# Optimization experiments

Measured on AMD Instinct MI355X. Metric: run time of the kernel, lower is better.

The kernel has to match this reference:

```python
import jax, jax.numpy as jnp
import numpy as np
from jax import lax

R = 0.1  # radius_graph radius (matches init kwarg r)


def setup_inputs() -> dict:
    key = jax.random.key(0)
    ks = jax.random.split(key, 16)
    B, O, K, F = 8, 4, 512, 3
    H = 128
    def lin(k, fan_in, fan_out):
        return jax.random.normal(k, (fan_in, fan_out), jnp.float32) / np.sqrt(fan_in)
    return {
        "points": jax.random.uniform(ks[0], (B, O, K, F), jnp.float32),
        "com": jax.random.normal(ks[1], (B, O, 3), jnp.float32),
        "com_vel": jax.random.normal(ks[2], (B, O, 3), jnp.float32),
        "angle": jax.random.normal(ks[3], (B, O, 3), jnp.float32),
        "angle_vel": jax.random.normal(ks[4], (B, O, 3), jnp.float32),
        "padding": jnp.ones((B, O, K), jnp.float32),
        "W0": lin(ks[5], 2 * F, H), "b0": jnp.zeros((H,), jnp.float32),
        "W1": lin(ks[6], H, H), "b1": jnp.zeros((H,), jnp.float32),
        "W2": lin(ks[7], H, H), "b2": jnp.zeros((H,), jnp.float32),
        "Wfc": lin(ks[8], H, 2 * F), "bfc": jnp.zeros((2 * F,), jnp.float32),
        "knn": 8,
        "pred_len": 10,
    }


def reference(points, com, com_vel, angle, angle_vel, padding,
              W0, b0, W1, b1, W2, b2, Wfc, bfc, knn, pred_len):
    B, O, K, F = points.shape
    N = O * K  # nodes per batch element
    pad = padding.reshape(B, N)                       # float mask [B,N]
    padb = pad > 0
    edge_ok = padb[:, :, None] & padb[:, None, :]     # valid src & dst
    not_self = ~jnp.eye(N, dtype=bool)
    eye = jnp.eye(N, dtype=points.dtype)

    states0 = jnp.concatenate([points, jnp.zeros_like(points)], -1).reshape(B, N, 2 * F)

    def gconv(a_hat, dinv, x, W, b):
        # GCNConv: out_i = sum_j A_hat[ij] d_i^-1/2 d_j^-1/2 (xW)_j + b
        h = (x @ W) * dinv[..., None]
        return jnp.einsum('bij,bjd->bid', a_hat, h) * dinv[..., None] + b

    def step(states, _):
        pos = states[..., :3]                         # [B,N,3]
        d2 = jnp.sum((pos[:, :, None, :] - pos[:, None, :, :]) ** 2, -1)
        adj = (d2 < R * R) & not_self & edge_ok       # radius_graph + padding mask
        a_hat = lax.stop_gradient(adj.astype(states.dtype) + eye)  # self-loops (all nodes)
        dinv = lax.rsqrt(a_hat.sum(-1))               # deg >= 1
        x = jax.nn.relu(gconv(a_hat, dinv, states, W0, b0))
        x = jax.nn.relu(gconv(a_hat, dinv, x, W1, b1))
        x = jax.nn.relu(gconv(a_hat, dinv, x, W2, b2))
        res = x @ Wfc + bfc
        new = states + res * pad[..., None]
        return new, new

    _, traj = lax.scan(step, states0, None, length=pred_len)
    traj = jnp.concatenate([states0[:, None], jnp.swapaxes(traj, 0, 1)], axis=1)
    return traj.reshape(B, pred_len + 1, O, K, 2 * F)[..., :3]
```

## Files before the change

### kernel.cpp

```cpp
#include <hip/hip_runtime.h>
#include <math.h>

#define BB 8
#define NN 2048
#define HH 128
#define NSEG 8
#define SEGJ 256
#define SEGCAP 12
#define MAXNBR (NSEG*SEGCAP)
#define PREDL 10
#define TSTRIDE (NN*3)
#define OUT_BSTRIDE ((PREDL+1)*NN*3)

__global__ __launch_bounds__(256) void k_init(const float* __restrict__ points,
                                              float* __restrict__ states,
                                              float* __restrict__ out) {
    int idx = blockIdx.x * 256 + threadIdx.x;
    if (idx >= BB * NN) return;
    int b = idx >> 11;
    int n = idx & 2047;
    float px = points[idx * 3 + 0];
    float py = points[idx * 3 + 1];
    float pz = points[idx * 3 + 2];
    float* s = states + (size_t)idx * 6;
    s[0] = px; s[1] = py; s[2] = pz; s[3] = 0.f; s[4] = 0.f; s[5] = 0.f;
    float* o = out + (size_t)b * OUT_BSTRIDE + n * 3;
    o[0] = px; o[1] = py; o[2] = pz;
}

__global__ __launch_bounds__(256, 2) void k_adj(const float* __restrict__ states,
                                                float* __restrict__ xs0,
                                                float* __restrict__ dinv,
                                                int* __restrict__ nbr,
                                                int* __restrict__ cntN) {
    const float R2c = 0.01f;
    int b = blockIdx.x & 7;
    int tile = blockIdx.x >> 3;
    __shared__ float4 pos[NN];
    __shared__ int degs[256];
    __shared__ unsigned short jb[256][SEGCAP];
    const float* sb = states + (size_t)b * NN * 6;
    for (int j = threadIdx.x; j < NN; j += 256) {
        const float* r = sb + j * 6;
        pos[j] = make_float4(r[0], r[1], r[2], 0.f);
    }
    __syncthreads();
    int node = threadIdx.x & 31;
    int seg  = threadIdx.x >> 5;
    int i = tile * 32 + node;
    int gi = b * NN + i;
    float4 pi = pos[i];
    int cnt = 0;
    int j0 = seg * SEGJ;
#pragma unroll 4
    for (int j = j0; j < j0 + SEGJ; ++j) {
        float4 pj = pos[j];
        float dx = pi.x - pj.x;
        float dy = pi.y - pj.y;
        float dz = pi.z - pj.z;
        float d2 = __fadd_rn(__fadd_rn(__fmul_rn(dx, dx), __fmul_rn(dy, dy)),
                             __fmul_rn(dz, dz));
        if (d2 < R2c && j != i) {
            if (cnt < SEGCAP) jb[threadIdx.x][cnt] = (unsigned short)j;
            cnt++;
        }
    }
    if (cnt > SEGCAP) cnt = SEGCAP;
    degs[threadIdx.x] = cnt;
    __syncthreads();
    int off = 0;
    for (int s = 0; s < seg; ++s) off += degs[s * 32 + node];
    int base = gi * MAXNBR + off;
    for (int k = 0; k < cnt; ++k) nbr[base + k] = (int)jb[threadIdx.x][k];
    if (seg == NSEG - 1) {
        int tot = off + cnt;
        cntN[gi] = tot;
        float di = (float)(1.0 / sqrt((double)(1 + tot)));
        dinv[gi] = di;
        const float* srow = sb + (size_t)i * 6;
        float* xr = xs0 + (size_t)gi * 6;
#pragma unroll
        for (int c = 0; c < 6; ++c) xr[c] = di * srow[c];
    }
}

__global__ __launch_bounds__(256, 2) void k_l0(const float* __restrict__ xs0,
                                               const float* __restrict__ dinv,
                                               const int* __restrict__ nbr,
                                               const int* __restrict__ cntN,
                                               const float* __restrict__ W0,
                                               const float* __restrict__ b0,
                                               float* __restrict__ xs1) {
    int b = blockIdx.x & 7;
    int tile = blockIdx.x >> 3;
    int node = threadIdx.x >> 3;
    int part = threadIdx.x & 7;
    int i = tile * 32 + node;
    int gi = b * NN + i;
    float g[6];
    {
        const float* sr = xs0 + (size_t)gi * 6;
        float2 a0 = *(const float2*)sr;
        float2 a1 = *(const float2*)(sr + 2);
        float2 a2 = *(const float2*)(sr + 4);
        g[0] = a0.x; g[1] = a0.y; g[2] = a1.x; g[3] = a1.y; g[4] = a2.x; g[5] = a2.y;
    }
    int cnt = cntN[gi];
    const int* nb = nbr + gi * MAXNBR;
    for (int k = 0; k < cnt; ++k) {
        int j = nb[k];
        const float* xr = xs0 + (size_t)(b * NN + j) * 6;
        float2 v0 = *(const float2*)xr;
        float2 v1 = *(const float2*)(xr + 2);
        float2 v2 = *(const float2*)(xr + 4);
        g[0] += v0.x; g[1] += v0.y; g[2] += v1.x;
        g[3] += v1.y; g[4] += v2.x; g[5] += v2.y;
    }
    float di = dinv[gi];
#pragma unroll
    for (int c = 0; c < 6; ++c) g[c] *= di;
    int c0 = part * 16;
    float y[16];
#pragma unroll
    for (int r = 0; r < 4; ++r) {
        float4 bv = *(const float4*)(b0 + c0 + r * 4);
        y[r * 4 + 0] = bv.x; y[r * 4 + 1] = bv.y; y[r * 4 + 2] = bv.z; y[r * 4 + 3] = bv.w;
    }
#pragma unroll
    for (int k = 0; k < 6; ++k) {
        float u = g[k];
        const float* wr = W0 + k * HH + c0;
#pragma unroll
        for (int r = 0; r < 4; ++r) {
            float4 w = *(const float4*)(wr + r * 4);
            y[r * 4 + 0] = fmaf(u, w.x, y[r * 4 + 0]);
            y[r * 4 + 1] = fmaf(u, w.y, y[r * 4 + 1]);
            y[r * 4 + 2] = fmaf(u, w.z, y[r * 4 + 2]);
            y[r * 4 + 3] = fmaf(u, w.w, y[r * 4 + 3]);
        }
    }
    float* xo = xs1 + (size_t)gi * HH + c0;
#pragma unroll
    for (int r = 0; r < 4; ++r) {
        float4 v;
        v.x = di * fmaxf(y[r * 4 + 0], 0.f);
        v.y = di * fmaxf(y[r * 4 + 1], 0.f);
        v.z = di * fmaxf(y[r * 4 + 2], 0.f);
        v.w = di * fmaxf(y[r * 4 + 3], 0.f);
        *(float4*)(xo + r * 4) = v;
    }
}

__device__ __forceinline__ void gather_into_lds(const float* __restrict__ xin,
                                                const float* __restrict__ dinv,
                                                const int* __restrict__ nbr,
                                                const int* __restrict__ cntN,
                                                int b, int tile,
                                                float (*uS)[HH + 4]) {
    const int node = threadIdx.x >> 3;
    const int part = threadIdx.x & 7;
    const int i = tile * 32 + node;
    const int gi = b * NN + i;
    const int c0 = part * 16;
    float acc[16];
    const float* xs = xin + (size_t)gi * HH + c0;
#pragma unroll
    for (int r = 0; r < 4; ++r) *(float4*)&acc[r * 4] = *(const float4*)(xs + r * 4);
    const int cnt = cntN[gi];
    const int* nb = nbr + gi * MAXNBR;
    for (int k = 0; k < cnt; ++k) {
        const int j = nb[k];
        const float* xr = xin + (size_t)(b * NN + j) * HH + c0;
#pragma unroll
        for (int r = 0; r < 4; ++r) {
            float v[4];
            *(float4*)v = *(const float4*)(xr + r * 4);
            acc[r * 4 + 0] += v[0]; acc[r * 4 + 1] += v[1];
            acc[r * 4 + 2] += v[2]; acc[r * 4 + 3] += v[3];
        }
    }
    const float di = dinv[gi];
#pragma unroll
    for (int r = 0; r < 4; ++r) {
        float4 o;
        o.x = acc[r * 4 + 0] * di; o.y = acc[r * 4 + 1] * di;
        o.z = acc[r * 4 + 2] * di; o.w = acc[r * 4 + 3] * di;
        *(float4*)&uS[node][c0 + r * 4] = o;
    }
}

__device__ __forceinline__ void gemm_panel(const float (*uS)[HH + 4],
                                           const float* __restrict__ wbuf,
                                           int p, int n0, int cA,
                                           float y0[8], float y1[8]) {
#pragma unroll 2
    for (int r = 0; r < 32; r += 4) {
        float ua[4], ub[4];
        *(float4*)ua = *(const float4*)(&uS[n0][p * 32 + r]);
        *(float4*)ub = *(const float4*)(&uS[n0 + 1][p * 32 + r]);
        const float* wrow = wbuf + r * HH + cA;
#pragma unroll
        for (int q = 0; q < 4; ++q) {
            float4 wa = *(const float4*)(wrow + q * HH);
            float4 wb = *(const float4*)(wrow + q * HH + 64);
            float u0 = ua[q], u1 = ub[q];
            y0[0] = fmaf(u0, wa.x, y0[0]); y0[1] = fmaf(u0, wa.y, y0[1]);
            y0[2] = fmaf(u0, wa.z, y0[2]); y0[3] = fmaf(u0, wa.w, y0[3]);
            y0[4] = fmaf(u0, wb.x, y0[4]); y0[5] = fmaf(u0, wb.y, y0[5]);
            y0[6] = fmaf(u0, wb.z, y0[6]); y0[7] = fmaf(u0, wb.w, y0[7]);
            y1[0] = fmaf(u1, wa.x, y1[0]); y1[1] = fmaf(u1, wa.y, y1[1]);
            y1[2] = fmaf(u1, wa.z, y1[2]); y1[3] = fmaf(u1, wa.w, y1[3]);
            y1[4] = fmaf(u1, wb.x, y1[4]); y1[5] = fmaf(u1, wb.y, y1[5]);
            y1[6] = fmaf(u1, wb.z, y1[6]); y1[7] = fmaf(u1, wb.w, y1[7]);
        }
    }
}

__global__ __launch_bounds__(256, 3) void k_mid(const float* __restrict__ xin,
                                                const float* __restrict__ dinv,
                                                const int* __restrict__ nbr,
                                                const int* __restrict__ cntN,
                                                const float* __restrict__ W,
                                                const float* __restrict__ bias,
                                                float* __restrict__ xout) {
    __shared__ __align__(16) float uS[32][HH + 4];
    __shared__ __align__(16) float wS[2][32 * HH];
    int b = blockIdx.x & 7;
    int tile = blockIdx.x >> 3;
    int t = threadIdx.x;
    const float4* Wf4 = (const float4*)W;
    float4 wreg[4];
#pragma unroll
    for (int q = 0; q < 4; ++q) wreg[q] = Wf4[t + q * 256];
    gather_into_lds(xin, dinv, nbr, cntN, b, tile, uS);
    {
        float4* ws4 = (float4*)wS[0];
#pragma unroll
        for (int q = 0; q < 4; ++q) ws4[t + q * 256] = wreg[q];
    }
    __syncthreads();
    int cb = t & 15, ng = t >> 4;
    int n0 = ng * 2, cA = cb * 4;
    float y0[8], y1[8];
    {
        float4 bv0 = *(const float4*)(bias + cA);
        float4 bv1 = *(const float4*)(bias + cA + 64);
        y0[0] = bv0.x; y0[1] = bv0.y; y0[2] = bv0.z; y0[3] = bv0.w;
        y0[4] = bv1.x; y0[5] = bv1.y; y0[6] = bv1.z; y0[7] = bv1.w;
#pragma unroll
        for (int r = 0; r < 8; ++r) y1[r] = y0[r];
    }
#pragma unroll
    for (int p = 0; p < 4; ++p) {
        if (p < 3) {
#pragma unroll
            for (int q = 0; q < 4; ++q) wreg[q] = Wf4[(p + 1) * 1024 + t + q * 256];
        }
        gemm_panel(uS, wS[p & 1], p, n0, cA, y0, y1);
        if (p < 3) {
            float4* ws4 = (float4*)wS[1 - (p & 1)];
#pragma unroll
            for (int q = 0; q < 4; ++q) ws4[t + q * 256] = wreg[q];
            __syncthreads();
        }
    }
    int g0 = b * NN + tile * 32 + n0;
    float di0 = dinv[g0], di1 = dinv[g0 + 1];
    float* o0 = xout + (size_t)g0 * HH + cA;
    float* o1 = o0 + HH;
    float4 va, vb;
    va.x = di0 * fmaxf(y0[0], 0.f); va.y = di0 * fmaxf(y0[1], 0.f);
    va.z = di0 * fmaxf(y0[2], 0.f); va.w = di0 * fmaxf(y0[3], 0.f);
    vb.x = di0 * fmaxf(y0[4], 0.f); vb.y = di0 * fmaxf(y0[5], 0.f);
    vb.z = di0 * fmaxf(y0[6], 0.f); vb.w = di0 * fmaxf(y0[7], 0.f);
    *(float4*)o0 = va; *(float4*)(o0 + 64) = vb;
    va.x = di1 * fmaxf(y1[0], 0.f); va.y = di1 * fmaxf(y1[1], 0.f);
    va.z = di1 * fmaxf(y1[2], 0.f); va.w = di1 * fmaxf(y1[3], 0.f);
    vb.x = di1 * fmaxf(y1[4], 0.f); vb.y = di1 * fmaxf(y1[5], 0.f);
    vb.z = di1 * fmaxf(y1[6], 0.f); vb.w = di1 * fmaxf(y1[7], 0.f);
    *(float4*)o1 = va; *(float4*)(o1 + 64) = vb;
}

__global__ __launch_bounds__(256, 3) void k_last(const float* __restrict__ xin,
                                                 const float* __restrict__ dinv,
                                                 const int* __restrict__ nbr,
                                                 const int* __restrict__ cntN,
                                                 const float* __restrict__ W2,
                                                 const float* __restrict__ b2,
                                                 const float* __restrict__ Wfc,
                                                 const float* __restrict__ bfc,
                                                 const float* __restrict__ padding,
                                                 float* __restrict__ states,
                                                 float* __restrict__ outt) {
    __shared__ __align__(16) float uS[32][HH + 4];
    __shared__ __align__(16) float wS[2][32 * HH];
    int b = blockIdx.x & 7;
    int tile = blockIdx.x >> 3;
    int t = threadIdx.x;
    const float4* Wf4 = (const float4*)W2;
    float4 wreg[4];
#pragma unroll
    for (int q = 0; q < 4; ++q) wreg[q] = Wf4[t + q * 256];
    gather_into_lds(xin, dinv, nbr, cntN, b, tile, uS);
    {
        float4* ws4 = (float4*)wS[0];
#pragma unroll
        for (int q = 0; q < 4; ++q) ws4[t + q * 256] = wreg[q];
    }
    __syncthreads();
    int cb = t & 15, ng = t >> 4;
    int n0 = ng * 2, cA = cb * 4;
    float y0[8], y1[8];
    {
        float4 bv0 = *(const float4*)(b2 + cA);
        float4 bv1 = *(const float4*)(b2 + cA + 64);
        y0[0] = bv0.x; y0[1] = bv0.y; y0[2] = bv0.z; y0[3] = bv0.w;
        y0[4] = bv1.x; y0[5] = bv1.y; y0[6] = bv1.z; y0[7] = bv1.w;
#pragma unroll
        for (int r = 0; r < 8; ++r) y1[r] = y0[r];
    }
#pragma unroll
    for (int p = 0; p < 4; ++p) {
        if (p < 3) {
#pragma unroll
            for (int q = 0; q < 4; ++q) wreg[q] = Wf4[(p + 1) * 1024 + t + q * 256];
        }
        gemm_panel(uS, wS[p & 1], p, n0, cA, y0, y1);
        if (p < 3) {
            float4* ws4 = (float4*)wS[1 - (p & 1)];
#pragma unroll
            for (int q = 0; q < 4; ++q) ws4[t + q * 256] = wreg[q];
            __syncthreads();
        }
    }
    __syncthreads();
    float* y3  = wS[0];
    float* wfc = wS[1];
#pragma unroll
    for (int q = 0; q < 3; ++q) wfc[t + q * 256] = Wfc[t + q * 256];
    {
        float4 v;
        v.x = fmaxf(y0[0], 0.f); v.y = fmaxf(y0[1], 0.f);
        v.z = fmaxf(y0[2], 0.f); v.w = fmaxf(y0[3], 0.f);
        *(float4*)&y3[n0 * HH + cA] = v;
        v.x = fmaxf(y0[4], 0.f); v.y = fmaxf(y0[5], 0.f);
        v.z = fmaxf(y0[6], 0.f); v.w = fmaxf(y0[7], 0.f);
        *(float4*)&y3[n0 * HH + cA + 64] = v;
        v.x = fmaxf(y1[0], 0.f); v.y = fmaxf(y1[1], 0.f);
        v.z = fmaxf(y1[2], 0.f); v.w = fmaxf(y1[3], 0.f);
        *(float4*)&y3[(n0 + 1) * HH + cA] = v;
        v.x = fmaxf(y1[4], 0.f); v.y = fmaxf(y1[5], 0.f);
        v.z = fmaxf(y1[6], 0.f); v.w = fmaxf(y1[7], 0.f);
        *(float4*)&y3[(n0 + 1) * HH + cA + 64] = v;
    }
    __syncthreads();
    if (t < 192) {
        int n = t / 6;
        int c = t - n * 6;
        float r = bfc[c];
        for (int k = 0; k < HH; k += 4) {
            float yv[4];
            *(float4*)yv = *(const float4*)&y3[n * HH + k];
            r = fmaf(yv[0], wfc[(k + 0) * 6 + c], r);
            r = fmaf(yv[1], wfc[(k + 1) * 6 + c], r);
            r = fmaf(yv[2], wfc[(k + 2) * 6 + c], r);
            r = fmaf(yv[3], wfc[(k + 3) * 6 + c], r);
        }
        int i = tile * 32 + n;
        int gi = b * NN + i;
        float pv = padding[b * NN + i];
        float s = states[(size_t)gi * 6 + c] + r * pv;
        states[(size_t)gi * 6 + c] = s;
        if (c < 3) outt[(size_t)b * OUT_BSTRIDE + i * 3 + c] = s;
    }
}

extern "C" void kernel_launch(void* const* d_in, const int* in_sizes, int n_in,
                              void* d_out, int out_size, void* d_ws, size_t ws_size,
                              hipStream_t stream) {
    (void)in_sizes; (void)n_in; (void)out_size; (void)ws_size;
    const float* points  = (const float*)d_in[0];
    const float* padding = (const float*)d_in[5];
    const float* W0  = (const float*)d_in[6];
    const float* b0  = (const float*)d_in[7];
    const float* W1  = (const float*)d_in[8];
    const float* b1  = (const float*)d_in[9];
    const float* W2  = (const float*)d_in[10];
    const float* b2  = (const float*)d_in[11];
    const float* Wfc = (const float*)d_in[12];
    const float* bfc = (const float*)d_in[13];
    float* out = (float*)d_out;

    float* ws     = (float*)d_ws;
    float* states = ws;
    float* xs0    = states + BB * NN * 6;
    float* xs1    = xs0 + BB * NN * 6;
    float* xs2    = xs1 + BB * NN * HH;
    float* dinvp  = xs2 + BB * NN * HH;
    int*   nbr    = (int*)(dinvp + BB * NN);
    int*   cntN   = nbr + BB * NN * MAXNBR;

    k_init<<<(BB * NN) / 256, 256, 0, stream>>>(points, states, out);
    for (int t = 0; t < PREDL; ++t) {
        k_adj<<<512, 256, 0, stream>>>(states, xs0, dinvp, nbr, cntN);
        k_l0<<<512, 256, 0, stream>>>(xs0, dinvp, nbr, cntN, W0, b0, xs1);
        k_mid<<<512, 256, 0, stream>>>(xs1, dinvp, nbr, cntN, W1, b1, xs2);
        k_last<<<512, 256, 0, stream>>>(xs2, dinvp, nbr, cntN, W2, b2, Wfc, bfc,
                                        padding, states,
                                        out + (size_t)(t + 1) * TSTRIDE);
    }
}
```

Before: 796.8 us.

## Fuse layer-0 into layer-1 kernel via recomputed two-hop gather, use 64-node tiles

Merges the layer-0 GCN kernel into the layer-1 kernel. Each block recomputes layer-0 outputs for every neighbor, doing a two-hop gather over the 6-wide inputs instead of writing and rereading the 128-wide xs1 buffer. This removes one launch per step and the xs1 round trip through global memory, in exchange for redundant layer-0 work per neighbor. All kernels also move to 512-thread blocks with 64 nodes per tile, which halves the grid to 256 blocks and roughly doubles LDS use per block.

New measurement: 1.536 ms. +92.8%, slower.

```diff
diff --git a/kernel.cpp b/kernel.cpp
--- a/kernel.cpp
+++ b/kernel.cpp
@@ -11,6 +11,7 @@
 #define PREDL 10
 #define TSTRIDE (NN*3)
 #define OUT_BSTRIDE ((PREDL+1)*NN*3)
+
 
 __global__ __launch_bounds__(256) void k_init(const float* __restrict__ points,
                                               float* __restrict__ states,
@@ -28,7 +29,7 @@
     o[0] = px; o[1] = py; o[2] = pz;
 }
 
-__global__ __launch_bounds__(256, 2) void k_adj(const float* __restrict__ states,
+__global__ __launch_bounds__(512, 2) void k_adj(const float* __restrict__ states,
                                                 float* __restrict__ xs0,
                                                 float* __restrict__ dinv,
                                                 int* __restrict__ nbr,
@@ -37,17 +38,17 @@
     int b = blockIdx.x & 7;
     int tile = blockIdx.x >> 3;
     __shared__ float4 pos[NN];
-    __shared__ int degs[256];
-    __shared__ unsigned short jb[256][SEGCAP];
+    __shared__ int degs[512];
+    __shared__ unsigned short jb[512][SEGCAP];
     const float* sb = states + (size_t)b * NN * 6;
-    for (int j = threadIdx.x; j < NN; j += 256) {
+    for (int j = threadIdx.x; j < NN; j += 512) {
         const float* r = sb + j * 6;
         pos[j] = make_float4(r[0], r[1], r[2], 0.f);
     }
     __syncthreads();
-    int node = threadIdx.x & 31;
-    int seg  = threadIdx.x >> 5;
-    int i = tile * 32 + node;
+    int node = threadIdx.x & 63;
+    int seg  = threadIdx.x >> 6;
+    int i = tile * 64 + node;
     int gi = b * NN + i;
     float4 pi = pos[i];
     int cnt = 0;
@@ -69,7 +70,7 @@
     degs[threadIdx.x] = cnt;
     __syncthreads();
     int off = 0;
-    for (int s = 0; s < seg; ++s) off += degs[s * 32 + node];
+    for (int s = 0; s < seg; ++s) off += degs[s * 64 + node];
     int base = gi * MAXNBR + off;
     for (int k = 0; k < cnt; ++k) nbr[base + k] = (int)jb[threadIdx.x][k];
     if (seg == NSEG - 1) {
@@ -81,111 +82,6 @@
         float* xr = xs0 + (size_t)gi * 6;
 #pragma unroll
         for (int c = 0; c < 6; ++c) xr[c] = di * srow[c];
-    }
-}
-
-__global__ __launch_bounds__(256, 2) void k_l0(const float* __restrict__ xs0,
-                                               const float* __restrict__ dinv,
-                                               const int* __restrict__ nbr,
-                                               const int* __restrict__ cntN,
-                                               const float* __restrict__ W0,
-                                               const float* __restrict__ b0,
-                                               float* __restrict__ xs1) {
-    int b = blockIdx.x & 7;
-    int tile = blockIdx.x >> 3;
-    int node = threadIdx.x >> 3;
-    int part = threadIdx.x & 7;
-    int i = tile * 32 + node;
-    int gi = b * NN + i;
-    float g[6];
-    {
-        const float* sr = xs0 + (size_t)gi * 6;
-        float2 a0 = *(const float2*)sr;
-        float2 a1 = *(const float2*)(sr + 2);
-        float2 a2 = *(const float2*)(sr + 4);
-        g[0] = a0.x; g[1] = a0.y; g[2] = a1.x; g[3] = a1.y; g[4] = a2.x; g[5] = a2.y;
-    }
-    int cnt = cntN[gi];
-    const int* nb = nbr + gi * MAXNBR;
-    for (int k = 0; k < cnt; ++k) {
-        int j = nb[k];
-        const float* xr = xs0 + (size_t)(b * NN + j) * 6;
-        float2 v0 = *(const float2*)xr;
-        float2 v1 = *(const float2*)(xr + 2);
-        float2 v2 = *(const float2*)(xr + 4);
-        g[0] += v0.x; g[1] += v0.y; g[2] += v1.x;
-        g[3] += v1.y; g[4] += v2.x; g[5] += v2.y;
-    }
-    float di = dinv[gi];
-#pragma unroll
-    for (int c = 0; c < 6; ++c) g[c] *= di;
-    int c0 = part * 16;
-    float y[16];
-#pragma unroll
-    for (int r = 0; r < 4; ++r) {
-        float4 bv = *(const float4*)(b0 + c0 + r * 4);
-        y[r * 4 + 0] = bv.x; y[r * 4 + 1] = bv.y; y[r * 4 + 2] = bv.z; y[r * 4 + 3] = bv.w;
-    }
-#pragma unroll
-    for (int k = 0; k < 6; ++k) {
-        float u = g[k];
-        const float* wr = W0 + k * HH + c0;
-#pragma unroll
-        for (int r = 0; r < 4; ++r) {
-            float4 w = *(const float4*)(wr + r * 4);
-            y[r * 4 + 0] = fmaf(u, w.x, y[r * 4 + 0]);
-            y[r * 4 + 1] = fmaf(u, w.y, y[r * 4 + 1]);
-            y[r * 4 + 2] = fmaf(u, w.z, y[r * 4 + 2]);
-            y[r * 4 + 3] = fmaf(u, w.w, y[r * 4 + 3]);
-        }
-    }
-    float* xo = xs1 + (size_t)gi * HH + c0;
-#pragma unroll
-    for (int r = 0; r < 4; ++r) {
-        float4 v;
-        v.x = di * fmaxf(y[r * 4 + 0], 0.f);
-        v.y = di * fmaxf(y[r * 4 + 1], 0.f);
-        v.z = di * fmaxf(y[r * 4 + 2], 0.f);
-        v.w = di * fmaxf(y[r * 4 + 3], 0.f);
-        *(float4*)(xo + r * 4) = v;
-    }
-}
-
-__device__ __forceinline__ void gather_into_lds(const float* __restrict__ xin,
-                                                const float* __restrict__ dinv,
-                                                const int* __restrict__ nbr,
-                                                const int* __restrict__ cntN,
-                                                int b, int tile,
-                                                float (*uS)[HH + 4]) {
-    const int node = threadIdx.x >> 3;
-    const int part = threadIdx.x & 7;
-    const int i = tile * 32 + node;
-    const int gi = b * NN + i;
-    const int c0 = part * 16;
-    float acc[16];
-    const float* xs = xin + (size_t)gi * HH + c0;
-#pragma unroll
-    for (int r = 0; r < 4; ++r) *(float4*)&acc[r * 4] = *(const float4*)(xs + r * 4);
-    const int cnt = cntN[gi];
-    const int* nb = nbr + gi * MAXNBR;
-    for (int k = 0; k < cnt; ++k) {
-        const int j = nb[k];
-        const float* xr = xin + (size_t)(b * NN + j) * HH + c0;
-#pragma unroll
-        for (int r = 0; r < 4; ++r) {
-            float v[4];
-            *(float4*)v = *(const float4*)(xr + r * 4);
-            acc[r * 4 + 0] += v[0]; acc[r * 4 + 1] += v[1];
-            acc[r * 4 + 2] += v[2]; acc[r * 4 + 3] += v[3];
-        }
-    }
-    const float di = dinv[gi];
-#pragma unroll
-    for (int r = 0; r < 4; ++r) {
-        float4 o;
-        o.x = acc[r * 4 + 0] * di; o.y = acc[r * 4 + 1] * di;
-        o.z = acc[r * 4 + 2] * di; o.w = acc[r * 4 + 3] * di;
-        *(float4*)&uS[node][c0 + r * 4] = o;
     }
 }
 
@@ -216,35 +112,115 @@
     }
 }
 
-__global__ __launch_bounds__(256, 3) void k_mid(const float* __restrict__ xin,
-                                                const float* __restrict__ dinv,
-                                                const int* __restrict__ nbr,
-                                                const int* __restrict__ cntN,
-                                                const float* __restrict__ W,
-                                                const float* __restrict__ bias,
-                                                float* __restrict__ xout) {
-    __shared__ __align__(16) float uS[32][HH + 4];
+__global__ __launch_bounds__(512, 2) void k_l0mid(
+    const float* __restrict__ xs0, const float* __restrict__ dinv,
+    const int* __restrict__ nbr, const int* __restrict__ cntN,
+    const float* __restrict__ W0, const float* __restrict__ b0v,
+    const float* __restrict__ W1, const float* __restrict__ b1v,
+    float* __restrict__ xs2)
+{
+    __shared__ __align__(16) float uS[64][HH + 4];
     __shared__ __align__(16) float wS[2][32 * HH];
+    __shared__ __align__(16) float w0S[800];
+    __shared__ __align__(16) float b0S[160];
+    int t = threadIdx.x;
     int b = blockIdx.x & 7;
     int tile = blockIdx.x >> 3;
-    int t = threadIdx.x;
-    const float4* Wf4 = (const float4*)W;
-    float4 wreg[4];
-#pragma unroll
-    for (int q = 0; q < 4; ++q) wreg[q] = Wf4[t + q * 256];
-    gather_into_lds(xin, dinv, nbr, cntN, b, tile, uS);
+    for (int q = t; q < 6 * HH; q += 512) {
+        int k = q >> 7, ch = q & 127;
+        w0S[(ch >> 4) * 100 + k * 16 + (ch & 15)] = W0[q];
+    }
+    if (t < HH) b0S[(t >> 4) * 20 + (t & 15)] = b0v[t];
+    const float4* Wf4 = (const float4*)W1;
+    float4 wreg[2];
+    wreg[0] = Wf4[t]; wreg[1] = Wf4[t + 512];
+    __syncthreads();
+
+    const int node = t >> 3;
+    const int part = t & 7;
+    const int c0 = part * 16;
+    const int i = tile * 64 + node;
+    const int gi = b * NN + i;
+    const float* w0p = w0S + part * 100;
+    const float* b0p = b0S + part * 20;
+    const float di_i = dinv[gi];
+    const int cnt_i = cntN[gi];
+    const int* nbi = nbr + (size_t)gi * MAXNBR;
+    float acc[16];
+    for (int idx = 0; idx <= cnt_i; ++idx) {
+        const int gv = (idx == 0) ? gi : (b * NN + nbi[idx - 1]);
+        float g[6];
+        {
+            const float* sr = xs0 + (size_t)gv * 6;
+            float2 a0 = *(const float2*)sr;
+            float2 a1 = *(const float2*)(sr + 2);
+            float2 a2 = *(const float2*)(sr + 4);
+            g[0] = a0.x; g[1] = a0.y; g[2] = a1.x;
+            g[3] = a1.y; g[4] = a2.x; g[5] = a2.y;
+        }
+        const int cv = cntN[gv];
+        const int* nb2 = nbr + (size_t)gv * MAXNBR;
+        for (int k = 0; k < cv; ++k) {
+            int j2 = nb2[k];
+            const float* xr = xs0 + (size_t)(b * NN + j2) * 6;
+            float2 v0 = *(const float2*)xr;
+            float2 v1 = *(const float2*)(xr + 2);
+            float2 v2 = *(const float2*)(xr + 4);
+            g[0] += v0.x; g[1] += v0.y; g[2] += v1.x;
+            g[3] += v1.y; g[4] += v2.x; g[5] += v2.y;
+        }
+        const float dv = dinv[gv];
+#pragma unroll
+        for (int c = 0; c < 6; ++c) g[c] *= dv;
+        float y[16];
+#pragma unroll
+        for (int r = 0; r < 4; ++r) {
+            float4 bv = *(const float4*)(b0p + r * 4);
+            y[r * 4 + 0] = bv.x; y[r * 4 + 1] = bv.y;
+            y[r * 4 + 2] = bv.z; y[r * 4 + 3] = bv.w;
+        }
+#pragma unroll
+        for (int k = 0; k < 6; ++k) {
+            float u = g[k];
+            const float* wr = w0p + k * 16;
+#pragma unroll
+            for (int r = 0; r < 4; ++r) {
+                float4 w = *(const float4*)(wr + r * 4);
+                y[r * 4 + 0] = fmaf(u, w.x, y[r * 4 + 0]);
+                y[r * 4 + 1] = fmaf(u, w.y, y[r * 4 + 1]);
+                y[r * 4 + 2] = fmaf(u, w.z, y[r * 4 + 2]);
+                y[r * 4 + 3] = fmaf(u, w.w, y[r * 4 + 3]);
+            }
+        }
+        if (idx == 0) {
+#pragma unroll
+            for (int e = 0; e < 16; ++e) acc[e] = __fmul_rn(dv, fmaxf(y[e], 0.f));
+        } else {
+#pragma unroll
+            for (int e = 0; e < 16; ++e)
+                acc[e] = __fadd_rn(acc[e], __fmul_rn(dv, fmaxf(y[e], 0.f)));
+        }
+    }
+#pragma unroll
+    for (int r = 0; r < 4; ++r) {
+        float4 o;
+        o.x = __fmul_rn(acc[r * 4 + 0], di_i);
+        o.y = __fmul_rn(acc[r * 4 + 1], di_i);
+        o.z = __fmul_rn(acc[r * 4 + 2], di_i);
+        o.w = __fmul_rn(acc[r * 4 + 3], di_i);
+        *(float4*)&uS[node][c0 + r * 4] = o;
+    }
     {
         float4* ws4 = (float4*)wS[0];
-#pragma unroll
-        for (int q = 0; q < 4; ++q) ws4[t + q * 256] = wreg[q];
+        ws4[t] = wreg[0]; ws4[t + 512] = wreg[1];
     }
     __syncthreads();
     int cb = t & 15, ng = t >> 4;
     int n0 = ng * 2, cA = cb * 4;
     float y0[8], y1[8];
     {
-        float4 bv0 = *(const float4*)(bias + cA);
-        float4 bv1 = *(const float4*)(bias + cA + 64);
+        float4 bv0 = *(const float4*)(b1v + cA);
+        float4 bv1 = *(const float4*)(b1v + cA + 64);
         y0[0] = bv0.x; y0[1] = bv0.y; y0[2] = bv0.z; y0[3] = bv0.w;
         y0[4] = bv1.x; y0[5] = bv1.y; y0[6] = bv1.z; y0[7] = bv1.w;
 #pragma unroll
@@ -253,20 +229,19 @@
 #pragma unroll
     for (int p = 0; p < 4; ++p) {
         if (p < 3) {
-#pragma unroll
-            for (int q = 0; q < 4; ++q) wreg[q] = Wf4[(p + 1) * 1024 + t + q * 256];
+            wreg[0] = Wf4[(p + 1) * 1024 + t];
+            wreg[1] = Wf4[(p + 1) * 1024 + t + 512];
         }
         gemm_panel(uS, wS[p & 1], p, n0, cA, y0, y1);
         if (p < 3) {
             float4* ws4 = (float4*)wS[1 - (p & 1)];
-#pragma unroll
-            for (int q = 0; q < 4; ++q) ws4[t + q * 256] = wreg[q];
+            ws4[t] = wreg[0]; ws4[t + 512] = wreg[1];
             __syncthreads();
         }
     }
-    int g0 = b * NN + tile * 32 + n0;
+    int g0 = b * NN + tile * 64 + n0;
     float di0 = dinv[g0], di1 = dinv[g0 + 1];
-    float* o0 = xout + (size_t)g0 * HH + cA;
+    float* o0 = xs2 + (size_t)g0 * HH + cA;
     float* o1 = o0 + HH;
     float4 va, vb;
     va.x = di0 * fmaxf(y0[0], 0.f); va.y = di0 * fmaxf(y0[1], 0.f);
@@ -281,7 +256,7 @@
     *(float4*)o1 = va; *(float4*)(o1 + 64) = vb;
 }
 
-__global__ __launch_bounds__(256, 3) void k_last(const float* __restrict__ xin,
+__global__ __launch_bounds__(512, 2) void k_last(const float* __restrict__ xin,
                                                  const float* __restrict__ dinv,
                                                  const int* __restrict__ nbr,
                                                  const int* __restrict__ cntN,
@@ -292,20 +267,51 @@
                                                  const float* __restrict__ padding,
                                                  float* __restrict__ states,
                                                  float* __restrict__ outt) {
-    __shared__ __align__(16) float uS[32][HH + 4];
+    __shared__ __align__(16) float uS[64][HH + 4];
     __shared__ __align__(16) float wS[2][32 * HH];
+    __shared__ __align__(16) float wfcS[HH * 6];
+    int t = threadIdx.x;
     int b = blockIdx.x & 7;
     int tile = blockIdx.x >> 3;
-    int t = threadIdx.x;
     const float4* Wf4 = (const float4*)W2;
-    float4 wreg[4];
-#pragma unroll
-    for (int q = 0; q < 4; ++q) wreg[q] = Wf4[t + q * 256];
-    gather_into_lds(xin, dinv, nbr, cntN, b, tile, uS);
+    float4 wreg[2];
+    wreg[0] = Wf4[t]; wreg[1] = Wf4[t + 512];
+    for (int q = t; q < HH * 6; q += 512) wfcS[q] = Wfc[q];
+    {
+        const int node = t >> 3;
+        const int part = t & 7;
+        const int i = tile * 64 + node;
+        const int gi = b * NN + i;
+        const int c0 = part * 16;
+        float acc[16];
+        const float* xs = xin + (size_t)gi * HH + c0;
+#pragma unroll
+        for (int r = 0; r < 4; ++r) *(float4*)&acc[r * 4] = *(const float4*)(xs + r * 4);
+        const int cnt = cntN[gi];
+        const int* nb = nbr + (size_t)gi * MAXNBR;
+        for (int k = 0; k < cnt; ++k) {
+            const int j = nb[k];
+            const float* xr = xin + (size_t)(b * NN + j) * HH + c0;
+#pragma unroll
+            for (int r = 0; r < 4; ++r) {
+                float v[4];
+                *(float4*)v = *(const float4*)(xr + r * 4);
+                acc[r * 4 + 0] += v[0]; acc[r * 4 + 1] += v[1];
+                acc[r * 4 + 2] += v[2]; acc[r * 4 + 3] += v[3];
+            }
+        }
+        const float di = dinv[gi];
+#pragma unroll
+        for (int r = 0; r < 4; ++r) {
+            float4 o;
+            o.x = acc[r * 4 + 0] * di; o.y = acc[r * 4 + 1] * di;
+            o.z = acc[r * 4 + 2] * di; o.w = acc[r * 4 + 3] * di;
+            *(float4*)&uS[node][c0 + r * 4] = o;
+        }
+    }
     {
         float4* ws4 = (float4*)wS[0];
-#pragma unroll
-        for (int q = 0; q < 4; ++q) ws4[t + q * 256] = wreg[q];
+        ws4[t] = wreg[0]; ws4[t + 512] = wreg[1];
     }
     __syncthreads();
     int cb = t & 15, ng = t >> 4;
@@ -322,51 +328,46 @@
 #pragma unroll
     for (int p = 0; p < 4; ++p) {
         if (p < 3) {
-#pragma unroll
-            for (int q = 0; q < 4; ++q) wreg[q] = Wf4[(p + 1) * 1024 + t + q * 256];
+            wreg[0] = Wf4[(p + 1) * 1024 + t];
+            wreg[1] = Wf4[(p + 1) * 1024 + t + 512];
         }
         gemm_panel(uS, wS[p & 1], p, n0, cA, y0, y1);
         if (p < 3) {
             float4* ws4 = (float4*)wS[1 - (p & 1)];
-#pragma unroll
-            for (int q = 0; q < 4; ++q) ws4[t + q * 256] = wreg[q];
+            ws4[t] = wreg[0]; ws4[t + 512] = wreg[1];
             __syncthreads();
         }
     }
     __syncthreads();
-    float* y3  = wS[0];
-    float* wfc = wS[1];
-#pragma unroll
-    for (int q = 0; q < 3; ++q) wfc[t + q * 256] = Wfc[t + q * 256];
     {
         float4 v;
         v.x = fmaxf(y0[0], 0.f); v.y = fmaxf(y0[1], 0.f);
         v.z = fmaxf(y0[2], 0.f); v.w = fmaxf(y0[3], 0.f);
-        *(float4*)&y3[n0 * HH + cA] = v;
+        *(float4*)&uS[n0][cA] = v;
         v.x = fmaxf(y0[4], 0.f); v.y = fmaxf(y0[5], 0.f);
         v.z = fmaxf(y0[6], 0.f); v.w = fmaxf(y0[7], 0.f);
-        *(float4*)&y3[n0 * HH + cA + 64] = v;
+        *(float4*)&uS[n0][cA + 64] = v;
         v.x = fmaxf(y1[0], 0.f); v.y = fmaxf(y1[1], 0.f);
         v.z = fmaxf(y1[2], 0.f); v.w = fmaxf(y1[3], 0.f);
-        *(float4*)&y3[(n0 + 1) * HH + cA] = v;
+        *(float4*)&uS[n0 + 1][cA] = v;
         v.x = fmaxf(y1[4], 0.f); v.y = fmaxf(y1[5], 0.f);
         v.z = fmaxf(y1[6], 0.f); v.w = fmaxf(y1[7], 0.f);
-        *(float4*)&y3[(n0 + 1) * HH + cA + 64] = v;
-    }
-    __syncthreads();
-    if (t < 192) {
+        *(float4*)&uS[n0 + 1][cA + 64] = v;
+    }
+    __syncthreads();
+    if (t < 384) {
         int n = t / 6;
         int c = t - n * 6;
         float r = bfc[c];
         for (int k = 0; k < HH; k += 4) {
             float yv[4];
-            *(float4*)yv = *(const float4*)&y3[n * HH + k];
-            r = fmaf(yv[0], wfc[(k + 0) * 6 + c], r);
-            r = fmaf(yv[1], wfc[(k + 1) * 6 + c], r);
-            r = fmaf(yv[2], wfc[(k + 2) * 6 + c], r);
-            r = fmaf(yv[3], wfc[(k + 3) * 6 + c], r);
-        }
-        int i = tile * 32 + n;
+            *(float4*)yv = *(const float4*)&uS[n][k];
+            r = fmaf(yv[0], wfcS[(k + 0) * 6 + c], r);
+            r = fmaf(yv[1], wfcS[(k + 1) * 6 + c], r);
+            r = fmaf(yv[2], wfcS[(k + 2) * 6 + c], r);
+            r = fmaf(yv[3], wfcS[(k + 3) * 6 + c], r);
+        }
+        int i = tile * 64 + n;
         int gi = b * NN + i;
         float pv = padding[b * NN + i];
         float s = states[(size_t)gi * 6 + c] + r * pv;
@@ -402,10 +403,9 @@
 
     k_init<<<(BB * NN) / 256, 256, 0, stream>>>(points, states, out);
     for (int t = 0; t < PREDL; ++t) {
-        k_adj<<<512, 256, 0, stream>>>(states, xs0, dinvp, nbr, cntN);
-        k_l0<<<512, 256, 0, stream>>>(xs0, dinvp, nbr, cntN, W0, b0, xs1);
-        k_mid<<<512, 256, 0, stream>>>(xs1, dinvp, nbr, cntN, W1, b1, xs2);
-        k_last<<<512, 256, 0, stream>>>(xs2, dinvp, nbr, cntN, W2, b2, Wfc, bfc,
+        k_adj<<<256, 512, 0, stream>>>(states, xs0, dinvp, nbr, cntN);
+        k_l0mid<<<256, 512, 0, stream>>>(xs0, dinvp, nbr, cntN, W0, b0, W1, b1, xs2);
+        k_last<<<256, 512, 0, stream>>>(xs2, dinvp, nbr, cntN, W2, b2, Wfc, bfc,
                                         padding, states,
                                         out + (size_t)(t + 1) * TSTRIDE);
     }
```

## Process 64 nodes per block in adjacency, mid and last GCN kernels

Applied to the files above, without the earlier changes.

Doubles the per-block node tile from 32 to 64 in k_adj, k_mid and k_last, halving the grid to 256 blocks. k_adj now tests each loaded position against two query nodes, which halves how often the position array is staged into LDS. The GEMM micro-tile grows to 4 nodes × 8 columns per thread, so each weight panel staged in LDS is reused across twice as many rows. The cost is more registers and LDS per block and only 256 blocks, about one per CU, so the GPU may be underfilled and less latency hiding is available.

After: 1.027 ms. +28.9%, slower.

```diff
diff --git a/kernel.cpp b/kernel.cpp
--- a/kernel.cpp
+++ b/kernel.cpp
@@ -11,6 +11,7 @@
 #define PREDL 10
 #define TSTRIDE (NN*3)
 #define OUT_BSTRIDE ((PREDL+1)*NN*3)
+
 
 __global__ __launch_bounds__(256) void k_init(const float* __restrict__ points,
                                               float* __restrict__ states,
@@ -37,8 +38,8 @@
     int b = blockIdx.x & 7;
     int tile = blockIdx.x >> 3;
     __shared__ float4 pos[NN];
-    __shared__ int degs[256];
-    __shared__ unsigned short jb[256][SEGCAP];
+    __shared__ int degs[2][256];
+    __shared__ unsigned short jb[2][256][SEGCAP];
     const float* sb = states + (size_t)b * NN * 6;
     for (int j = threadIdx.x; j < NN; j += 256) {
         const float* r = sb + j * 6;
@@ -47,40 +48,65 @@
     __syncthreads();
     int node = threadIdx.x & 31;
     int seg  = threadIdx.x >> 5;
-    int i = tile * 32 + node;
-    int gi = b * NN + i;
-    float4 pi = pos[i];
-    int cnt = 0;
+    int i1 = tile * 64 + node;
+    int i2 = i1 + 32;
+    int gi1 = b * NN + i1;
+    int gi2 = b * NN + i2;
+    float4 p1 = pos[i1];
+    float4 p2 = pos[i2];
+    int c1 = 0, c2 = 0;
     int j0 = seg * SEGJ;
-#pragma unroll 4
+#pragma unroll 2
     for (int j = j0; j < j0 + SEGJ; ++j) {
         float4 pj = pos[j];
-        float dx = pi.x - pj.x;
-        float dy = pi.y - pj.y;
-        float dz = pi.z - pj.z;
-        float d2 = __fadd_rn(__fadd_rn(__fmul_rn(dx, dx), __fmul_rn(dy, dy)),
-                             __fmul_rn(dz, dz));
-        if (d2 < R2c && j != i) {
-            if (cnt < SEGCAP) jb[threadIdx.x][cnt] = (unsigned short)j;
-            cnt++;
-        }
-    }
-    if (cnt > SEGCAP) cnt = SEGCAP;
-    degs[threadIdx.x] = cnt;
-    __syncthreads();
-    int off = 0;
-    for (int s = 0; s < seg; ++s) off += degs[s * 32 + node];
-    int base = gi * MAXNBR + off;
-    for (int k = 0; k < cnt; ++k) nbr[base + k] = (int)jb[threadIdx.x][k];
+        float dx1 = p1.x - pj.x, dy1 = p1.y - pj.y, dz1 = p1.z - pj.z;
+        float d21 = __fadd_rn(__fadd_rn(__fmul_rn(dx1, dx1), __fmul_rn(dy1, dy1)),
+                              __fmul_rn(dz1, dz1));
+        float dx2 = p2.x - pj.x, dy2 = p2.y - pj.y, dz2 = p2.z - pj.z;
+        float d22 = __fadd_rn(__fadd_rn(__fmul_rn(dx2, dx2), __fmul_rn(dy2, dy2)),
+                              __fmul_rn(dz2, dz2));
+        if (d21 < R2c && j != i1) {
+            if (c1 < SEGCAP) jb[0][threadIdx.x][c1] = (unsigned short)j;
+            c1++;
+        }
+        if (d22 < R2c && j != i2) {
+            if (c2 < SEGCAP) jb[1][threadIdx.x][c2] = (unsigned short)j;
+            c2++;
+        }
+    }
+    if (c1 > SEGCAP) c1 = SEGCAP;
+    if (c2 > SEGCAP) c2 = SEGCAP;
+    degs[0][threadIdx.x] = c1;
+    degs[1][threadIdx.x] = c2;
+    __syncthreads();
+    int off1 = 0, off2 = 0;
+    for (int s = 0; s < seg; ++s) {
+        off1 += degs[0][s * 32 + node];
+        off2 += degs[1][s * 32 + node];
+    }
+    {
+        int base1 = gi1 * MAXNBR + off1;
+        for (int k = 0; k < c1; ++k) nbr[base1 + k] = (int)jb[0][threadIdx.x][k];
+        int base2 = gi2 * MAXNBR + off2;
+        for (int k = 0; k < c2; ++k) nbr[base2 + k] = (int)jb[1][threadIdx.x][k];
+    }
     if (seg == NSEG - 1) {
-        int tot = off + cnt;
-        cntN[gi] = tot;
-        float di = (float)(1.0 / sqrt((double)(1 + tot)));
-        dinv[gi] = di;
-        const float* srow = sb + (size_t)i * 6;
-        float* xr = xs0 + (size_t)gi * 6;
-#pragma unroll
-        for (int c = 0; c < 6; ++c) xr[c] = di * srow[c];
+        int tot1 = off1 + c1;
+        int tot2 = off2 + c2;
+        cntN[gi1] = tot1;
+        cntN[gi2] = tot2;
+        float d1 = (float)(1.0 / sqrt((double)(1 + tot1)));
+        float d2v = (float)(1.0 / sqrt((double)(1 + tot2)));
+        dinv[gi1] = d1;
+        dinv[gi2] = d2v;
+        const float* s1 = sb + (size_t)i1 * 6;
+        const float* s2 = sb + (size_t)i2 * 6;
+        float* x1 = xs0 + (size_t)gi1 * 6;
+        float* x2 = xs0 + (size_t)gi2 * 6;
+#pragma unroll
+        for (int c = 0; c < 6; ++c) x1[c] = d1 * s1[c];
+#pragma unroll
+        for (int c = 0; c < 6; ++c) x2[c] = d2v * s2[c];
     }
 }
 
@@ -151,28 +177,29 @@
     }
 }
 
-__device__ __forceinline__ void gather_into_lds(const float* __restrict__ xin,
-                                                const float* __restrict__ dinv,
-                                                const int* __restrict__ nbr,
-                                                const int* __restrict__ cntN,
-                                                int b, int tile,
-                                                float (*uS)[HH + 4]) {
-    const int node = threadIdx.x >> 3;
-    const int part = threadIdx.x & 7;
-    const int i = tile * 32 + node;
+__device__ __forceinline__ void gather64(const float* __restrict__ xin,
+                                         const float* __restrict__ dinv,
+                                         const int* __restrict__ nbr,
+                                         const int* __restrict__ cntN,
+                                         int b, int tile,
+                                         float (*uS)[HH + 4]) {
+    const int t = threadIdx.x;
+    const int node = t >> 2;
+    const int part = t & 3;
+    const int c0 = part * 32;
+    const int i = tile * 64 + node;
     const int gi = b * NN + i;
-    const int c0 = part * 16;
-    float acc[16];
+    float acc[32];
     const float* xs = xin + (size_t)gi * HH + c0;
 #pragma unroll
-    for (int r = 0; r < 4; ++r) *(float4*)&acc[r * 4] = *(const float4*)(xs + r * 4);
+    for (int r = 0; r < 8; ++r) *(float4*)&acc[r * 4] = *(const float4*)(xs + r * 4);
     const int cnt = cntN[gi];
-    const int* nb = nbr + gi * MAXNBR;
+    const int* nb = nbr + (size_t)gi * MAXNBR;
     for (int k = 0; k < cnt; ++k) {
         const int j = nb[k];
         const float* xr = xin + (size_t)(b * NN + j) * HH + c0;
 #pragma unroll
-        for (int r = 0; r < 4; ++r) {
+        for (int r = 0; r < 8; ++r) {
             float v[4];
             *(float4*)v = *(const float4*)(xr + r * 4);
             acc[r * 4 + 0] += v[0]; acc[r * 4 + 1] += v[1];
@@ -181,7 +208,7 @@
     }
     const float di = dinv[gi];
 #pragma unroll
-    for (int r = 0; r < 4; ++r) {
+    for (int r = 0; r < 8; ++r) {
         float4 o;
         o.x = acc[r * 4 + 0] * di; o.y = acc[r * 4 + 1] * di;
         o.z = acc[r * 4 + 2] * di; o.w = acc[r * 4 + 3] * di;
@@ -189,41 +216,41 @@
     }
 }
 
-__device__ __forceinline__ void gemm_panel(const float (*uS)[HH + 4],
-                                           const float* __restrict__ wbuf,
-                                           int p, int n0, int cA,
-                                           float y0[8], float y1[8]) {
+__device__ __forceinline__ void gemm_panel4(const float (*uS)[HH + 4],
+                                            const float* __restrict__ wbuf,
+                                            int p, int n0, int cA,
+                                            float y[4][8]) {
 #pragma unroll 2
     for (int r = 0; r < 32; r += 4) {
-        float ua[4], ub[4];
-        *(float4*)ua = *(const float4*)(&uS[n0][p * 32 + r]);
-        *(float4*)ub = *(const float4*)(&uS[n0 + 1][p * 32 + r]);
+        float u[4][4];
+#pragma unroll
+        for (int n = 0; n < 4; ++n)
+            *(float4*)u[n] = *(const float4*)(&uS[n0 + n][p * 32 + r]);
         const float* wrow = wbuf + r * HH + cA;
 #pragma unroll
         for (int q = 0; q < 4; ++q) {
             float4 wa = *(const float4*)(wrow + q * HH);
             float4 wb = *(const float4*)(wrow + q * HH + 64);
-            float u0 = ua[q], u1 = ub[q];
-            y0[0] = fmaf(u0, wa.x, y0[0]); y0[1] = fmaf(u0, wa.y, y0[1]);
-            y0[2] = fmaf(u0, wa.z, y0[2]); y0[3] = fmaf(u0, wa.w, y0[3]);
-            y0[4] = fmaf(u0, wb.x, y0[4]); y0[5] = fmaf(u0, wb.y, y0[5]);
-            y0[6] = fmaf(u0, wb.z, y0[6]); y0[7] = fmaf(u0, wb.w, y0[7]);
-            y1[0] = fmaf(u1, wa.x, y1[0]); y1[1] = fmaf(u1, wa.y, y1[1]);
-            y1[2] = fmaf(u1, wa.z, y1[2]); y1[3] = fmaf(u1, wa.w, y1[3]);
-            y1[4] = fmaf(u1, wb.x, y1[4]); y1[5] = fmaf(u1, wb.y, y1[5]);
-            y1[6] = fmaf(u1, wb.z, y1[6]); y1[7] = fmaf(u1, wb.w, y1[7]);
-        }
-    }
-}
-
-__global__ __launch_bounds__(256, 3) void k_mid(const float* __restrict__ xin,
+#pragma unroll
+            for (int n = 0; n < 4; ++n) {
+                float uu = u[n][q];
+                y[n][0] = fmaf(uu, wa.x, y[n][0]); y[n][1] = fmaf(uu, wa.y, y[n][1]);
+                y[n][2] = fmaf(uu, wa.z, y[n][2]); y[n][3] = fmaf(uu, wa.w, y[n][3]);
+                y[n][4] = fmaf(uu, wb.x, y[n][4]); y[n][5] = fmaf(uu, wb.y, y[n][5]);
+                y[n][6] = fmaf(uu, wb.z, y[n][6]); y[n][7] = fmaf(uu, wb.w, y[n][7]);
+            }
+        }
+    }
+}
+
+__global__ __launch_bounds__(256, 2) void k_mid(const float* __restrict__ xin,
                                                 const float* __restrict__ dinv,
                                                 const int* __restrict__ nbr,
                                                 const int* __restrict__ cntN,
                                                 const float* __restrict__ W,
                                                 const float* __restrict__ bias,
                                                 float* __restrict__ xout) {
-    __shared__ __align__(16) float uS[32][HH + 4];
+    __shared__ __align__(16) float uS[64][HH + 4];
     __shared__ __align__(16) float wS[2][32 * HH];
     int b = blockIdx.x & 7;
     int tile = blockIdx.x >> 3;
@@ -232,7 +259,7 @@
     float4 wreg[4];
 #pragma unroll
     for (int q = 0; q < 4; ++q) wreg[q] = Wf4[t + q * 256];
-    gather_into_lds(xin, dinv, nbr, cntN, b, tile, uS);
+    gather64(xin, dinv, nbr, cntN, b, tile, uS);
     {
         float4* ws4 = (float4*)wS[0];
 #pragma unroll
@@ -240,15 +267,16 @@
     }
     __syncthreads();
     int cb = t & 15, ng = t >> 4;
-    int n0 = ng * 2, cA = cb * 4;
-    float y0[8], y1[8];
+    int n0 = ng * 4, cA = cb * 4;
+    float y[4][8];
     {
         float4 bv0 = *(const float4*)(bias + cA);
         float4 bv1 = *(const float4*)(bias + cA + 64);
-        y0[0] = bv0.x; y0[1] = bv0.y; y0[2] = bv0.z; y0[3] = bv0.w;
-        y0[4] = bv1.x; y0[5] = bv1.y; y0[6] = bv1.z; y0[7] = bv1.w;
-#pragma unroll
-        for (int r = 0; r < 8; ++r) y1[r] = y0[r];
+#pragma unroll
+        for (int n = 0; n < 4; ++n) {
+            y[n][0] = bv0.x; y[n][1] = bv0.y; y[n][2] = bv0.z; y[n][3] = bv0.w;
+            y[n][4] = bv1.x; y[n][5] = bv1.y; y[n][6] = bv1.z; y[n][7] = bv1.w;
+        }
     }
 #pragma unroll
     for (int p = 0; p < 4; ++p) {
@@ -256,7 +284,7 @@
 #pragma unroll
             for (int q = 0; q < 4; ++q) wreg[q] = Wf4[(p + 1) * 1024 + t + q * 256];
         }
-        gemm_panel(uS, wS[p & 1], p, n0, cA, y0, y1);
+        gemm_panel4(uS, wS[p & 1], p, n0, cA, y);
         if (p < 3) {
             float4* ws4 = (float4*)wS[1 - (p & 1)];
 #pragma unroll
@@ -264,24 +292,21 @@
             __syncthreads();
         }
     }
-    int g0 = b * NN + tile * 32 + n0;
-    float di0 = dinv[g0], di1 = dinv[g0 + 1];
-    float* o0 = xout + (size_t)g0 * HH + cA;
-    float* o1 = o0 + HH;
-    float4 va, vb;
-    va.x = di0 * fmaxf(y0[0], 0.f); va.y = di0 * fmaxf(y0[1], 0.f);
-    va.z = di0 * fmaxf(y0[2], 0.f); va.w = di0 * fmaxf(y0[3], 0.f);
-    vb.x = di0 * fmaxf(y0[4], 0.f); vb.y = di0 * fmaxf(y0[5], 0.f);
-    vb.z = di0 * fmaxf(y0[6], 0.f); vb.w = di0 * fmaxf(y0[7], 0.f);
-    *(float4*)o0 = va; *(float4*)(o0 + 64) = vb;
-    va.x = di1 * fmaxf(y1[0], 0.f); va.y = di1 * fmaxf(y1[1], 0.f);
-    va.z = di1 * fmaxf(y1[2], 0.f); va.w = di1 * fmaxf(y1[3], 0.f);
-    vb.x = di1 * fmaxf(y1[4], 0.f); vb.y = di1 * fmaxf(y1[5], 0.f);
-    vb.z = di1 * fmaxf(y1[6], 0.f); vb.w = di1 * fmaxf(y1[7], 0.f);
-    *(float4*)o1 = va; *(float4*)(o1 + 64) = vb;
-}
-
-__global__ __launch_bounds__(256, 3) void k_last(const float* __restrict__ xin,
+    int g0 = b * NN + tile * 64 + n0;
+#pragma unroll
+    for (int n = 0; n < 4; ++n) {
+        float di = dinv[g0 + n];
+        float* o = xout + (size_t)(g0 + n) * HH + cA;
+        float4 va, vb;
+        va.x = di * fmaxf(y[n][0], 0.f); va.y = di * fmaxf(y[n][1], 0.f);
+        va.z = di * fmaxf(y[n][2], 0.f); va.w = di * fmaxf(y[n][3], 0.f);
+        vb.x = di * fmaxf(y[n][4], 0.f); vb.y = di * fmaxf(y[n][5], 0.f);
+        vb.z = di * fmaxf(y[n][6], 0.f); vb.w = di * fmaxf(y[n][7], 0.f);
+        *(float4*)o = va; *(float4*)(o + 64) = vb;
+    }
+}
+
+__global__ __launch_bounds__(256, 2) void k_last(const float* __restrict__ xin,
                                                  const float* __restrict__ dinv,
                                                  const int* __restrict__ nbr,
                                                  const int* __restrict__ cntN,
@@ -292,8 +317,9 @@
                                                  const float* __restrict__ padding,
                                                  float* __restrict__ states,
                                                  float* __restrict__ outt) {
-    __shared__ __align__(16) float uS[32][HH + 4];
+    __shared__ __align__(16) float uS[64][HH + 4];
     __shared__ __align__(16) float wS[2][32 * HH];
+    __shared__ __align__(16) float wfcS[HH * 6];
     int b = blockIdx.x & 7;
     int tile = blockIdx.x >> 3;
     int t = threadIdx.x;
@@ -301,7 +327,8 @@
     float4 wreg[4];
 #pragma unroll
     for (int q = 0; q < 4; ++q) wreg[q] = Wf4[t + q * 256];
-    gather_into_lds(xin, dinv, nbr, cntN, b, tile, uS);
+    for (int q = t; q < HH * 6; q += 256) wfcS[q] = Wfc[q];
+    gather64(xin, dinv, nbr, cntN, b, tile, uS);
     {
         float4* ws4 = (float4*)wS[0];
 #pragma unroll
@@ -309,15 +336,16 @@
     }
     __syncthreads();
     int cb = t & 15, ng = t >> 4;
-    int n0 = ng * 2, cA = cb * 4;
-    float y0[8], y1[8];
+    int n0 = ng * 4, cA = cb * 4;
+    float y[4][8];
     {
         float4 bv0 = *(const float4*)(b2 + cA);
         float4 bv1 = *(const float4*)(b2 + cA + 64);
-        y0[0] = bv0.x; y0[1] = bv0.y; y0[2] = bv0.z; y0[3] = bv0.w;
-        y0[4] = bv1.x; y0[5] = bv1.y; y0[6] = bv1.z; y0[7] = bv1.w;
-#pragma unroll
-        for (int r = 0; r < 8; ++r) y1[r] = y0[r];
+#pragma unroll
+        for (int n = 0; n < 4; ++n) {
+            y[n][0] = bv0.x; y[n][1] = bv0.y; y[n][2] = bv0.z; y[n][3] = bv0.w;
+            y[n][4] = bv1.x; y[n][5] = bv1.y; y[n][6] = bv1.z; y[n][7] = bv1.w;
+        }
     }
 #pragma unroll
     for (int p = 0; p < 4; ++p) {
@@ -325,7 +353,7 @@
 #pragma unroll
             for (int q = 0; q < 4; ++q) wreg[q] = Wf4[(p + 1) * 1024 + t + q * 256];
         }
-        gemm_panel(uS, wS[p & 1], p, n0, cA, y0, y1);
+        gemm_panel4(uS, wS[p & 1], p, n0, cA, y);
         if (p < 3) {
             float4* ws4 = (float4*)wS[1 - (p & 1)];
 #pragma unroll
@@ -334,39 +362,30 @@
         }
     }
     __syncthreads();
-    float* y3  = wS[0];
-    float* wfc = wS[1];
-#pragma unroll
-    for (int q = 0; q < 3; ++q) wfc[t + q * 256] = Wfc[t + q * 256];
-    {
+#pragma unroll
+    for (int n = 0; n < 4; ++n) {
         float4 v;
-        v.x = fmaxf(y0[0], 0.f); v.y = fmaxf(y0[1], 0.f);
-        v.z = fmaxf(y0[2], 0.f); v.w = fmaxf(y0[3], 0.f);
-        *(float4*)&y3[n0 * HH + cA] = v;
-        v.x = fmaxf(y0[4], 0.f); v.y = fmaxf(y0[5], 0.f);
-        v.z = fmaxf(y0[6], 0.f); v.w = fmaxf(y0[7], 0.f);
-        *(float4*)&y3[n0 * HH + cA + 64] = v;
-        v.x = fmaxf(y1[0], 0.f); v.y = fmaxf(y1[1], 0.f);
-        v.z = fmaxf(y1[2], 0.f); v.w = fmaxf(y1[3], 0.f);
-        *(float4*)&y3[(n0 + 1) * HH + cA] = v;
-        v.x = fmaxf(y1[4], 0.f); v.y = fmaxf(y1[5], 0.f);
-        v.z = fmaxf(y1[6], 0.f); v.w = fmaxf(y1[7], 0.f);
-        *(float4*)&y3[(n0 + 1) * HH + cA + 64] = v;
-    }
-    __syncthreads();
-    if (t < 192) {
-        int n = t / 6;
-        int c = t - n * 6;
+        v.x = fmaxf(y[n][0], 0.f); v.y = fmaxf(y[n][1], 0.f);
+        v.z = fmaxf(y[n][2], 0.f); v.w = fmaxf(y[n][3], 0.f);
+        *(float4*)&uS[n0 + n][cA] = v;
+        v.x = fmaxf(y[n][4], 0.f); v.y = fmaxf(y[n][5], 0.f);
+        v.z = fmaxf(y[n][6], 0.f); v.w = fmaxf(y[n][7], 0.f);
+        *(float4*)&uS[n0 + n][cA + 64] = v;
+    }
+    __syncthreads();
+    for (int pq = t; pq < 384; pq += 256) {
+        int n = pq / 6;
+        int c = pq - n * 6;
         float r = bfc[c];
         for (int k = 0; k < HH; k += 4) {
             float yv[4];
-            *(float4*)yv = *(const float4*)&y3[n * HH + k];
-            r = fmaf(yv[0], wfc[(k + 0) * 6 + c], r);
-            r = fmaf(yv[1], wfc[(k + 1) * 6 + c], r);
-            r = fmaf(yv[2], wfc[(k + 2) * 6 + c], r);
-            r = fmaf(yv[3], wfc[(k + 3) * 6 + c], r);
-        }
-        int i = tile * 32 + n;
+            *(float4*)yv = *(const float4*)&uS[n][k];
+            r = fmaf(yv[0], wfcS[(k + 0) * 6 + c], r);
+            r = fmaf(yv[1], wfcS[(k + 1) * 6 + c], r);
+            r = fmaf(yv[2], wfcS[(k + 2) * 6 + c], r);
+            r = fmaf(yv[3], wfcS[(k + 3) * 6 + c], r);
+        }
+        int i = tile * 64 + n;
         int gi = b * NN + i;
         float pv = padding[b * NN + i];
         float s = states[(size_t)gi * 6 + c] + r * pv;
@@ -402,10 +421,10 @@
 
     k_init<<<(BB * NN) / 256, 256, 0, stream>>>(points, states, out);
     for (int t = 0; t < PREDL; ++t) {
-        k_adj<<<512, 256, 0, stream>>>(states, xs0, dinvp, nbr, cntN);
+        k_adj<<<256, 256, 0, stream>>>(states, xs0, dinvp, nbr, cntN);
         k_l0<<<512, 256, 0, stream>>>(xs0, dinvp, nbr, cntN, W0, b0, xs1);
-        k_mid<<<512, 256, 0, stream>>>(xs1, dinvp, nbr, cntN, W1, b1, xs2);
-        k_last<<<512, 256, 0, stream>>>(xs2, dinvp, nbr, cntN, W2, b2, Wfc, bfc,
+        k_mid<<<256, 256, 0, stream>>>(xs1, dinvp, nbr, cntN, W1, b1, xs2);
+        k_last<<<256, 256, 0, stream>>>(xs2, dinvp, nbr, cntN, W2, b2, Wfc, bfc,
                                         padding, states,
                                         out + (size_t)(t + 1) * TSTRIDE);
     }
```
